# Kernel tuning notes

Hardware: AMD Instinct MI355X
Metric: run time of the kernel (lower is better)

## Reference

```python
import jax, jax.numpy as jnp
import numpy as np

THR = 1.0  # snntorch Leaky default threshold

# Heaviside spike with ATan surrogate gradient (snntorch surrogate.atan, alpha=2)
@jax.custom_vjp
def atan_spike(x):
    return (x > 0).astype(x.dtype)

def _spike_fwd(x):
    return atan_spike(x), x

def _spike_bwd(x, g):
    # d/dx of surrogate: (alpha/2) / (1 + (pi/2*alpha*x)^2) with alpha=2 -> 1/(1+(pi*x)^2)
    return (g / (1.0 + (jnp.pi * x) ** 2),)

atan_spike.defvjp(_spike_fwd, _spike_bwd)


def setup_inputs() -> dict:
    key = jax.random.key(0)
    ks = jax.random.split(key, 5)
    B, T = 256, 100
    D, H, O = 34 * 34 * 2, 1000, 10
    data = jax.random.normal(ks[0], (B, T, 2, 34, 34), jnp.float32)
    lim1 = 1.0 / np.sqrt(D)
    lim2 = 1.0 / np.sqrt(H)
    w1 = jax.random.uniform(ks[1], (H, D), jnp.float32, -lim1, lim1)
    b1 = jax.random.uniform(ks[2], (H,), jnp.float32, -lim1, lim1)
    w2 = jax.random.uniform(ks[3], (O, H), jnp.float32, -lim2, lim2)
    b2 = jax.random.uniform(ks[4], (O,), jnp.float32, -lim2, lim2)
    beta = jnp.float32(0.9)
    return {"data": data, "w1": w1, "b1": b1, "w2": w2, "b2": b2, "beta": beta}


def reference(data, w1, b1, w2, b2, beta):
    B, T = data.shape[0], data.shape[1]
    H, O = w1.shape[0], w2.shape[0]
    x = data.reshape(B, T, -1).transpose(1, 0, 2)  # [T, B, D] (Flatten per step)
    # Input currents to layer 1 are state-independent: one batched GEMM.
    cur1_all = jnp.einsum('tbd,hd->tbh', x, w1) + b1  # [T, B, H]

    mem1 = jnp.zeros((B, H), data.dtype)
    spk1 = jnp.zeros((B, H), data.dtype)
    mem2 = jnp.zeros((B, O), data.dtype)
    spk2 = jnp.zeros((B, O), data.dtype)

    def step(carry, cur1):
        mem1, spk1, mem2, spk2 = carry
        # snntorch Leaky, reset_mechanism='subtract':
        # mem = beta*mem + input - reset*threshold ; spk = fire(mem)
        mem1 = beta * mem1 + cur1 - spk1 * THR
        spk1 = atan_spike(mem1 - THR)
        cur2 = spk1 @ w2.T + b2
        mem2 = beta * mem2 + cur2 - spk2 * THR
        spk2 = atan_spike(mem2 - THR)
        return (mem1, spk1, mem2, spk2), (spk2, mem2)

    _, (spk_rec, mem_rec) = jax.lax.scan(step, (mem1, spk1, mem2, spk2), cur1_all)
    return spk_rec, mem_rec  # each [T, B, 10]
```

## Files before the change

kernel.cpp:

```cpp
#include <hip/hip_runtime.h>
#include <hip/hip_bf16.h>
#include <stdint.h>

#define T_STEPS 100
#define B_SZ    256
#define D_IN    2312
#define H_SZ    1000
#define O_SZ    10
#define M_ROWS  (B_SZ * T_STEPS)
#define K_PAD   2336
#define KT      73
#define W_ROWS  1024

#define A_SCALE   16.0f
#define W_SCALE   64.0f
#define INV_SCALE (1.0f / 1024.0f)

typedef __attribute__((ext_vector_type(4))) float     floatx4;
typedef __attribute__((ext_vector_type(8))) _Float16  halfx8;

#define ASYNC_COPY16(g, l)                                             \
  __builtin_amdgcn_global_load_lds(                                    \
      (const __attribute__((address_space(1))) void*)(g),              \
      (__attribute__((address_space(3))) void*)(l), 16, 0, 0)

__global__ __launch_bounds__(256)
void splitW_kernel(const float* __restrict__ W,
                   _Float16* __restrict__ wHi,
                   _Float16* __restrict__ wLo)
{
  const int r = blockIdx.x;
  const bool rvalid = (r < H_SZ);
  const float* w = W + (size_t)(rvalid ? r : 0) * D_IN;
  _Float16* ho = wHi + (size_t)r * K_PAD;
  _Float16* lo = wLo + (size_t)r * K_PAD;
  for (int c = threadIdx.x; c < K_PAD / 8; c += 256) {
    const int k0 = c * 8;
    const bool v = rvalid && (k0 + 8 <= D_IN);
    _Float16 h[8], l[8];
    #pragma unroll
    for (int e = 0; e < 8; ++e) {
      const float x = v ? w[k0 + e] * W_SCALE : 0.f;
      const _Float16 hb = (_Float16)x;
      h[e] = hb;
      l[e] = (_Float16)(x - (float)hb);
    }
    *reinterpret_cast<uint4*>(ho + k0) = *reinterpret_cast<const uint4*>(h);
    *reinterpret_cast<uint4*>(lo + k0) = *reinterpret_cast<const uint4*>(l);
  }
}

__global__ __launch_bounds__(256)
void gemm1_fused(const float* __restrict__ A,
                 const _Float16* __restrict__ wHi,
                 const _Float16* __restrict__ wLo,
                 const float* __restrict__ b1,
                 float* __restrict__ C)
{
  __shared__ _Float16 sAh[128 * 32];
  __shared__ _Float16 sAl[128 * 32];
  __shared__ _Float16 sBh[2][128 * 32];
  __shared__ _Float16 sBl[2][128 * 32];

  const int tid  = threadIdx.x;

  const int id  = blockIdx.x;
  const int j   = id >> 3;
  const int mt  = (id & 7) * 25 + (j >> 3);
  const int nt  = j & 7;
  const int m0  = mt * 128;
  const int n0  = nt * 128;

  const int wid  = tid >> 6;
  const int lane = tid & 63;
  const int wm   = (wid & 1) * 64;
  const int wn   = (wid >> 1) * 64;
  const int quad = lane >> 4;
  const int l16  = lane & 15;

  floatx4 acc[4][4];
  #pragma unroll
  for (int i = 0; i < 4; ++i)
    #pragma unroll
    for (int jj = 0; jj < 4; ++jj)
      acc[i][jj] = floatx4{0.f, 0.f, 0.f, 0.f};

  const int r0  = tid >> 2;
  const int r1  = r0 + 64;
  const int sl  = tid & 3;
  const int rho = (r0 >> 1) & 3;
  const int ko  = ((sl ^ rho) * 8);

  const float* gA0 = A + (size_t)(m0 + r0) * D_IN + ko;
  const float* gA1 = A + (size_t)(m0 + r1) * D_IN + ko;
  const _Float16* gBh0 = wHi + (size_t)(n0 + r0) * K_PAD + ko;
  const _Float16* gBh1 = wHi + (size_t)(n0 + r1) * K_PAD + ko;
  const _Float16* gBl0 = wLo + (size_t)(n0 + r0) * K_PAD + ko;
  const _Float16* gBl1 = wLo + (size_t)(n0 + r1) * K_PAD + ko;

  _Float16* lAh0 = sAh + (size_t)tid * 8;
  _Float16* lAh1 = sAh + (size_t)(tid + 256) * 8;
  _Float16* lAl0 = sAl + (size_t)tid * 8;
  _Float16* lAl1 = sAl + (size_t)(tid + 256) * 8;
  const int lb0 = tid * 8;
  const int lb1 = (tid + 256) * 8;

  const int fo = (quad ^ ((l16 >> 1) & 3)) * 8;

  float a0[8], a1[8];
  *reinterpret_cast<float4*>(a0)     = *reinterpret_cast<const float4*>(gA0);
  *reinterpret_cast<float4*>(a0 + 4) = *reinterpret_cast<const float4*>(gA0 + 4);
  *reinterpret_cast<float4*>(a1)     = *reinterpret_cast<const float4*>(gA1);
  *reinterpret_cast<float4*>(a1 + 4) = *reinterpret_cast<const float4*>(gA1 + 4);
  bool curValid = true;

  ASYNC_COPY16(gBh0, &sBh[0][lb0]);
  ASYNC_COPY16(gBh1, &sBh[0][lb1]);
  ASYNC_COPY16(gBl0, &sBl[0][lb0]);
  ASYNC_COPY16(gBl1, &sBl[0][lb1]);

  for (int kt = 0; kt < KT; ++kt) {
    const int p = kt & 1;

    {
      _Float16 h0[8], l0[8], h1[8], l1[8];
      #pragma unroll
      for (int e = 0; e < 8; ++e) {
        const float v0 = curValid ? a0[e] * A_SCALE : 0.f;
        const _Float16 hb0 = (_Float16)v0;
        h0[e] = hb0; l0[e] = (_Float16)(v0 - (float)hb0);
        const float v1 = curValid ? a1[e] * A_SCALE : 0.f;
        const _Float16 hb1 = (_Float16)v1;
        h1[e] = hb1; l1[e] = (_Float16)(v1 - (float)hb1);
      }
      *reinterpret_cast<uint4*>(lAh0) = *reinterpret_cast<const uint4*>(h0);
      *reinterpret_cast<uint4*>(lAl0) = *reinterpret_cast<const uint4*>(l0);
      *reinterpret_cast<uint4*>(lAh1) = *reinterpret_cast<const uint4*>(h1);
      *reinterpret_cast<uint4*>(lAl1) = *reinterpret_cast<const uint4*>(l1);
    }

    if (kt + 1 < KT) {
      const int kb = (kt + 1) * 32;
      const bool v = (kb + ko) < D_IN;
      const int off = v ? kb : 0;
      *reinterpret_cast<float4*>(a0)     = *reinterpret_cast<const float4*>(gA0 + off);
      *reinterpret_cast<float4*>(a0 + 4) = *reinterpret_cast<const float4*>(gA0 + off + 4);
      *reinterpret_cast<float4*>(a1)     = *reinterpret_cast<const float4*>(gA1 + off);
      *reinterpret_cast<float4*>(a1 + 4) = *reinterpret_cast<const float4*>(gA1 + off + 4);
      curValid = v;
      ASYNC_COPY16(gBh0 + kb, &sBh[p ^ 1][lb0]);
      ASYNC_COPY16(gBh1 + kb, &sBh[p ^ 1][lb1]);
      ASYNC_COPY16(gBl0 + kb, &sBl[p ^ 1][lb0]);
      ASYNC_COPY16(gBl1 + kb, &sBl[p ^ 1][lb1]);
      asm volatile("s_waitcnt vmcnt(8) lgkmcnt(0)" ::: "memory");
    } else {
      asm volatile("s_waitcnt vmcnt(0) lgkmcnt(0)" ::: "memory");
    }
    __builtin_amdgcn_s_barrier();
    asm volatile("" ::: "memory");

    halfx8 ah[4], bh[4], al[4], bl[4];
    #pragma unroll
    for (int i = 0; i < 4; ++i) {
      const int row = (wm + i * 16 + l16) * 32 + fo;
      ah[i] = *reinterpret_cast<const halfx8*>(sAh + row);
      al[i] = *reinterpret_cast<const halfx8*>(sAl + row);
    }
    #pragma unroll
    for (int jj = 0; jj < 4; ++jj) {
      const int row = (wn + jj * 16 + l16) * 32 + fo;
      bh[jj] = *reinterpret_cast<const halfx8*>(&sBh[p][row]);
      bl[jj] = *reinterpret_cast<const halfx8*>(&sBl[p][row]);
    }
    #pragma unroll
    for (int i = 0; i < 4; ++i)
      #pragma unroll
      for (int jj = 0; jj < 4; ++jj)
        acc[i][jj] = __builtin_amdgcn_mfma_f32_16x16x32_f16(ah[i], bh[jj], acc[i][jj], 0, 0, 0);
    #pragma unroll
    for (int i = 0; i < 4; ++i)
      #pragma unroll
      for (int jj = 0; jj < 4; ++jj)
        acc[i][jj] = __builtin_amdgcn_mfma_f32_16x16x32_f16(al[i], bh[jj], acc[i][jj], 0, 0, 0);
    #pragma unroll
    for (int i = 0; i < 4; ++i)
      #pragma unroll
      for (int jj = 0; jj < 4; ++jj)
        acc[i][jj] = __builtin_amdgcn_mfma_f32_16x16x32_f16(ah[i], bl[jj], acc[i][jj], 0, 0, 0);

    asm volatile("" ::: "memory");
    __builtin_amdgcn_s_barrier();
    asm volatile("" ::: "memory");
  }

  #pragma unroll
  for (int jj = 0; jj < 4; ++jj) {
    const int col = n0 + wn + jj * 16 + l16;
    if (col < H_SZ) {
      const float bias = b1[col];
      #pragma unroll
      for (int i = 0; i < 4; ++i) {
        const int row = m0 + wm + i * 16 + quad * 4;
        #pragma unroll
        for (int r = 0; r < 4; ++r)
          C[(size_t)(row + r) * H_SZ + col] = acc[i][jj][r] * INV_SCALE + bias;
      }
    }
  }
}

__global__ __launch_bounds__(256)
void scan1_kernel(const float* __restrict__ cur1,
                  const float* __restrict__ beta_p,
                  __hip_bfloat16* __restrict__ spk1)
{
  const int h = blockIdx.x * 256 + threadIdx.x;
  const int b = blockIdx.y;
  if (h >= H_SZ) return;
  const float beta = beta_p[0];
  const float* c    = cur1 + (size_t)b * T_STEPS * H_SZ + h;
  __hip_bfloat16* s = spk1 + (size_t)b * T_STEPS * H_SZ + h;
  float mem = 0.f, spk = 0.f;
  #pragma unroll 4
  for (int t = 0; t < T_STEPS; ++t) {
    mem = beta * mem + c[(size_t)t * H_SZ] - spk;
    spk = (mem > 1.0f) ? 1.0f : 0.0f;
    s[(size_t)t * H_SZ] = __float2bfloat16(spk);
  }
}

__global__ __launch_bounds__(256)
void gemm2_kernel(const __hip_bfloat16* __restrict__ spk1,
                  const float* __restrict__ w2,
                  float* __restrict__ cur2)
{
  const int wid  = threadIdx.x >> 6;
  const int lane = threadIdx.x & 63;
  const int m    = blockIdx.x * 4 + wid;

  float acc[O_SZ];
  #pragma unroll
  for (int o = 0; o < O_SZ; ++o) acc[o] = 0.f;

  const __hip_bfloat16* row = spk1 + (size_t)m * H_SZ;
  #pragma unroll
  for (int it = 0; it < 16; ++it) {
    const int h = it * 64 + lane;
    if (h < H_SZ) {
      const float s = __bfloat162float(row[h]);
      if (s != 0.f) {
        #pragma unroll
        for (int o = 0; o < O_SZ; ++o)
          acc[o] += w2[o * H_SZ + h];
      }
    }
  }
  #pragma unroll
  for (int o = 0; o < O_SZ; ++o) {
    float v = acc[o];
    #pragma unroll
    for (int off = 32; off > 0; off >>= 1) v += __shfl_down(v, off);
    if (lane == 0) cur2[(size_t)m * O_SZ + o] = v;
  }
}

__global__ __launch_bounds__(256)
void scan2_kernel(const float* __restrict__ cur2,
                  const float* __restrict__ b2,
                  const float* __restrict__ beta_p,
                  float* __restrict__ out)
{
  const int idx = blockIdx.x * 256 + threadIdx.x;
  if (idx >= B_SZ * O_SZ) return;
  const int b = idx / O_SZ;
  const int o = idx % O_SZ;
  const float beta = beta_p[0];
  const float bias = b2[o];
  float* spk_rec = out;
  float* mem_rec = out + (size_t)T_STEPS * B_SZ * O_SZ;
  float mem = 0.f, spk = 0.f;
  for (int t = 0; t < T_STEPS; ++t) {
    const float cur = cur2[((size_t)b * T_STEPS + t) * O_SZ + o] + bias;
    mem = beta * mem + cur - spk;
    spk = (mem > 1.0f) ? 1.0f : 0.0f;
    const size_t oi = ((size_t)t * B_SZ + b) * O_SZ + o;
    spk_rec[oi] = spk;
    mem_rec[oi] = mem;
  }
}

extern "C" void kernel_launch(void* const* d_in, const int* in_sizes, int n_in,
                              void* d_out, int out_size, void* d_ws, size_t ws_size,
                              hipStream_t stream)
{
  const float* data = (const float*)d_in[0];
  const float* w1   = (const float*)d_in[1];
  const float* b1   = (const float*)d_in[2];
  const float* w2   = (const float*)d_in[3];
  const float* b2   = (const float*)d_in[4];
  const float* beta = (const float*)d_in[5];
  float* out = (float*)d_out;

  char* p = (char*)d_ws;
  auto take = [&](size_t n) { char* q = p; p += (n + 255) & ~(size_t)255; return q; };
  _Float16*       wHi  = (_Float16*)take((size_t)W_ROWS * K_PAD * 2);
  _Float16*       wLo  = (_Float16*)take((size_t)W_ROWS * K_PAD * 2);
  float*          cur1 = (float*)take((size_t)M_ROWS * H_SZ * 4);
  __hip_bfloat16* spk1 = (__hip_bfloat16*)take((size_t)M_ROWS * H_SZ * 2);
  float*          cur2 = (float*)take((size_t)M_ROWS * O_SZ * 4);

  splitW_kernel<<<dim3(W_ROWS), 256, 0, stream>>>(w1, wHi, wLo);
  gemm1_fused<<<dim3(1600), 256, 0, stream>>>(data, wHi, wLo, b1, cur1);
  scan1_kernel<<<dim3(4, B_SZ), 256, 0, stream>>>(cur1, beta, spk1);
  gemm2_kernel<<<dim3(M_ROWS / 4), 256, 0, stream>>>(spk1, w2, cur2);
  scan2_kernel<<<dim3(10), 256, 0, stream>>>(cur2, b2, beta, out);
}
```

Baseline: 911.9 us.

## Double-buffer A tile in LDS and use a single barrier per k-step

```diff
diff --git a/kernel.cpp b/kernel.cpp
--- a/kernel.cpp
+++ b/kernel.cpp
@@ -57,8 +57,8 @@
                  const float* __restrict__ b1,
                  float* __restrict__ C)
 {
-  __shared__ _Float16 sAh[128 * 32];
-  __shared__ _Float16 sAl[128 * 32];
+  __shared__ _Float16 sAh[2][128 * 32];
+  __shared__ _Float16 sAl[2][128 * 32];
   __shared__ _Float16 sBh[2][128 * 32];
   __shared__ _Float16 sBl[2][128 * 32];
 
@@ -98,12 +98,8 @@
   const _Float16* gBl0 = wLo + (size_t)(n0 + r0) * K_PAD + ko;
   const _Float16* gBl1 = wLo + (size_t)(n0 + r1) * K_PAD + ko;
 
-  _Float16* lAh0 = sAh + (size_t)tid * 8;
-  _Float16* lAh1 = sAh + (size_t)(tid + 256) * 8;
-  _Float16* lAl0 = sAl + (size_t)tid * 8;
-  _Float16* lAl1 = sAl + (size_t)(tid + 256) * 8;
-  const int lb0 = tid * 8;
-  const int lb1 = (tid + 256) * 8;
+  const int la0 = tid * 8;
+  const int la1 = (tid + 256) * 8;
 
   const int fo = (quad ^ ((l16 >> 1) & 3)) * 8;
 
@@ -112,17 +108,55 @@
   *reinterpret_cast<float4*>(a0 + 4) = *reinterpret_cast<const float4*>(gA0 + 4);
   *reinterpret_cast<float4*>(a1)     = *reinterpret_cast<const float4*>(gA1);
   *reinterpret_cast<float4*>(a1 + 4) = *reinterpret_cast<const float4*>(gA1 + 4);
+
+  ASYNC_COPY16(gBh0, &sBh[0][la0]);
+  ASYNC_COPY16(gBh1, &sBh[0][la1]);
+  ASYNC_COPY16(gBl0, &sBl[0][la0]);
+  ASYNC_COPY16(gBl1, &sBl[0][la1]);
+
+  {
+    _Float16 h0[8], l0[8], h1[8], l1[8];
+    #pragma unroll
+    for (int e = 0; e < 8; ++e) {
+      const float v0 = a0[e] * A_SCALE;
+      const _Float16 hb0 = (_Float16)v0;
+      h0[e] = hb0; l0[e] = (_Float16)(v0 - (float)hb0);
+      const float v1 = a1[e] * A_SCALE;
+      const _Float16 hb1 = (_Float16)v1;
+      h1[e] = hb1; l1[e] = (_Float16)(v1 - (float)hb1);
+    }
+    *reinterpret_cast<uint4*>(&sAh[0][la0]) = *reinterpret_cast<const uint4*>(h0);
+    *reinterpret_cast<uint4*>(&sAl[0][la0]) = *reinterpret_cast<const uint4*>(l0);
+    *reinterpret_cast<uint4*>(&sAh[0][la1]) = *reinterpret_cast<const uint4*>(h1);
+    *reinterpret_cast<uint4*>(&sAl[0][la1]) = *reinterpret_cast<const uint4*>(l1);
+  }
+
+  *reinterpret_cast<float4*>(a0)     = *reinterpret_cast<const float4*>(gA0 + 32);
+  *reinterpret_cast<float4*>(a0 + 4) = *reinterpret_cast<const float4*>(gA0 + 36);
+  *reinterpret_cast<float4*>(a1)     = *reinterpret_cast<const float4*>(gA1 + 32);
+  *reinterpret_cast<float4*>(a1 + 4) = *reinterpret_cast<const float4*>(gA1 + 36);
   bool curValid = true;
-
-  ASYNC_COPY16(gBh0, &sBh[0][lb0]);
-  ASYNC_COPY16(gBh1, &sBh[0][lb1]);
-  ASYNC_COPY16(gBl0, &sBl[0][lb0]);
-  ASYNC_COPY16(gBl1, &sBl[0][lb1]);
 
   for (int kt = 0; kt < KT; ++kt) {
     const int p = kt & 1;
 
-    {
+    __syncthreads();
+
+    halfx8 ah[4], bh[4], al[4], bl[4];
+    #pragma unroll
+    for (int i = 0; i < 4; ++i) {
+      const int row = (wm + i * 16 + l16) * 32 + fo;
+      ah[i] = *reinterpret_cast<const halfx8*>(&sAh[p][row]);
+      al[i] = *reinterpret_cast<const halfx8*>(&sAl[p][row]);
+    }
+    #pragma unroll
+    for (int jj = 0; jj < 4; ++jj) {
+      const int row = (wn + jj * 16 + l16) * 32 + fo;
+      bh[jj] = *reinterpret_cast<const halfx8*>(&sBh[p][row]);
+      bl[jj] = *reinterpret_cast<const halfx8*>(&sBl[p][row]);
+    }
+
+    if (kt + 1 < KT) {
       _Float16 h0[8], l0[8], h1[8], l1[8];
       #pragma unroll
       for (int e = 0; e < 8; ++e) {
@@ -133,45 +167,30 @@
         const _Float16 hb1 = (_Float16)v1;
         h1[e] = hb1; l1[e] = (_Float16)(v1 - (float)hb1);
       }
-      *reinterpret_cast<uint4*>(lAh0) = *reinterpret_cast<const uint4*>(h0);
-      *reinterpret_cast<uint4*>(lAl0) = *reinterpret_cast<const uint4*>(l0);
-      *reinterpret_cast<uint4*>(lAh1) = *reinterpret_cast<const uint4*>(h1);
-      *reinterpret_cast<uint4*>(lAl1) = *reinterpret_cast<const uint4*>(l1);
-    }
-
-    if (kt + 1 < KT) {
+      const int q = p ^ 1;
+      *reinterpret_cast<uint4*>(&sAh[q][la0]) = *reinterpret_cast<const uint4*>(h0);
+      *reinterpret_cast<uint4*>(&sAl[q][la0]) = *reinterpret_cast<const uint4*>(l0);
+      *reinterpret_cast<uint4*>(&sAh[q][la1]) = *reinterpret_cast<const uint4*>(h1);
+      *reinterpret_cast<uint4*>(&sAl[q][la1]) = *reinterpret_cast<const uint4*>(l1);
+
       const int kb = (kt + 1) * 32;
-      const bool v = (kb + ko) < D_IN;
-      const int off = v ? kb : 0;
+      ASYNC_COPY16(gBh0 + kb, &sBh[q][la0]);
+      ASYNC_COPY16(gBh1 + kb, &sBh[q][la1]);
+      ASYNC_COPY16(gBl0 + kb, &sBl[q][la0]);
+      ASYNC_COPY16(gBl1 + kb, &sBl[q][la1]);
+    }
+
+    if (kt + 2 < KT) {
+      const int kb2 = (kt + 2) * 32;
+      const bool v = (kb2 + ko) < D_IN;
+      const int off = v ? kb2 : 0;
       *reinterpret_cast<float4*>(a0)     = *reinterpret_cast<const float4*>(gA0 + off);
       *reinterpret_cast<float4*>(a0 + 4) = *reinterpret_cast<const float4*>(gA0 + off + 4);
       *reinterpret_cast<float4*>(a1)     = *reinterpret_cast<const float4*>(gA1 + off);
       *reinterpret_cast<float4*>(a1 + 4) = *reinterpret_cast<const float4*>(gA1 + off + 4);
       curValid = v;
-      ASYNC_COPY16(gBh0 + kb, &sBh[p ^ 1][lb0]);
-      ASYNC_COPY16(gBh1 + kb, &sBh[p ^ 1][lb1]);
-      ASYNC_COPY16(gBl0 + kb, &sBl[p ^ 1][lb0]);
-      ASYNC_COPY16(gBl1 + kb, &sBl[p ^ 1][lb1]);
-      asm volatile("s_waitcnt vmcnt(8) lgkmcnt(0)" ::: "memory");
-    } else {
-      asm volatile("s_waitcnt vmcnt(0) lgkmcnt(0)" ::: "memory");
-    }
-    __builtin_amdgcn_s_barrier();
-    asm volatile("" ::: "memory");
-
-    halfx8 ah[4], bh[4], al[4], bl[4];
-    #pragma unroll
-    for (int i = 0; i < 4; ++i) {
-      const int row = (wm + i * 16 + l16) * 32 + fo;
-      ah[i] = *reinterpret_cast<const halfx8*>(sAh + row);
-      al[i] = *reinterpret_cast<const halfx8*>(sAl + row);
-    }
-    #pragma unroll
-    for (int jj = 0; jj < 4; ++jj) {
-      const int row = (wn + jj * 16 + l16) * 32 + fo;
-      bh[jj] = *reinterpret_cast<const halfx8*>(&sBh[p][row]);
-      bl[jj] = *reinterpret_cast<const halfx8*>(&sBl[p][row]);
-    }
+    }
+
     #pragma unroll
     for (int i = 0; i < 4; ++i)
       #pragma unroll
@@ -187,10 +206,6 @@
       #pragma unroll
       for (int jj = 0; jj < 4; ++jj)
         acc[i][jj] = __builtin_amdgcn_mfma_f32_16x16x32_f16(ah[i], bl[jj], acc[i][jj], 0, 0, 0);
-
-    asm volatile("" ::: "memory");
-    __builtin_amdgcn_s_barrier();
-    asm volatile("" ::: "memory");
   }
 
   #pragma unroll
```

New measurement: 821.0 us. 1.11x faster.
